# Kernel optimization log

Measured on AMD Instinct MI355X. Metric: run time of the kernel, lower is better.

The kernel has to match this reference:

```python
import jax, jax.numpy as jnp
import numpy as np

N_NODES = 100000
N_EDGES = 1600000
IN_N, IN_E = 128, 64
OUT_N, OUT_E, H = 16, 16, 4


def setup_inputs() -> dict:
    key = jax.random.key(0)
    ks = jax.random.split(key, 11)
    s = 0.05
    return {
        'nfeats': jax.random.normal(ks[0], (N_NODES, IN_N), jnp.float32),
        'efeats': jax.random.normal(ks[1], (N_EDGES, IN_E), jnp.float32),
        'src': jax.random.randint(ks[2], (N_EDGES,), 0, N_NODES, jnp.int32),
        'dst': jax.random.randint(ks[3], (N_EDGES,), 0, N_NODES, jnp.int32),
        'W_ni': jax.random.normal(ks[4], (IN_N, H * OUT_E), jnp.float32) * s,
        'W_nj': jax.random.normal(ks[5], (IN_N, H * OUT_E), jnp.float32) * s,
        'W_fij': jax.random.normal(ks[6], (IN_E, H * OUT_E), jnp.float32) * s,
        'W_src': jax.random.normal(ks[7], (IN_N, H * OUT_N), jnp.float32) * s,
        'b_src': jax.random.normal(ks[8], (H * OUT_N,), jnp.float32) * s,
        'attn': jax.random.normal(ks[9], (H, OUT_E), jnp.float32) * s,
        'bias_e': jax.random.normal(ks[10], (H * OUT_E,), jnp.float32) * s,
    }


def reference(nfeats, efeats, src, dst, W_ni, W_nj, W_fij, W_src, b_src, attn, bias_e):
    N = nfeats.shape[0]
    Hh, De = attn.shape
    # edge features: f_ij = leaky_relu(f_ni[src] + f_nj[dst] + fc_fij(efeats) + bias)
    f_ni = nfeats @ W_ni                                   # [N, H*De]
    f_nj = nfeats @ W_nj                                   # [N, H*De]
    f_fij = efeats @ W_fij                                 # [E, H*De]
    f_out = f_ni[src] + f_nj[dst] + f_fij + bias_e         # [E, H*De]
    f_out = jax.nn.leaky_relu(f_out, 0.01).reshape(-1, Hh, De)  # [E, H, De]
    # attention logits and per-destination softmax (edge_softmax)
    e = jnp.einsum('ehd,hd->eh', f_out, attn)              # [E, H]
    m = jax.ops.segment_max(e, dst, num_segments=N)        # [N, H]
    ex = jnp.exp(e - m[dst])
    z = jax.ops.segment_sum(ex, dst, num_segments=N)       # [N, H]
    a = ex / z[dst]                                        # [E, H]
    # message passing: sum_j a_ij * h_src_j
    h_src = (nfeats @ W_src + b_src).reshape(N, Hh, -1)    # [N, H, Dn]
    msg = a[:, :, None] * h_src[src]                       # [E, H, Dn]
    h_out = jax.ops.segment_sum(msg, dst, num_segments=N)  # [N, H, Dn]
    # aggr='mean' over heads
    res_n = h_out.mean(axis=-2)                            # [N, Dn]
    res_e = f_out.mean(axis=-2)                            # [E, De]
    return res_n, res_e
```

## Files before the change

kernel.cpp:

```cpp
#include <hip/hip_runtime.h>

#define N_NODES 100000
#define N_EDGES 1600000

typedef __bf16 bf16x8 __attribute__((ext_vector_type(8)));
typedef float f32x4 __attribute__((ext_vector_type(4)));

__device__ __forceinline__ __bf16 f2bf(float f) { return (__bf16)f; }

__device__ __forceinline__ bf16x8 cvt8(float4 a, float4 b) {
    bf16x8 r;
    r[0] = f2bf(a.x); r[1] = f2bf(a.y); r[2] = f2bf(a.z); r[3] = f2bf(a.w);
    r[4] = f2bf(b.x); r[5] = f2bf(b.y); r[6] = f2bf(b.z); r[7] = f2bf(b.w);
    return r;
}

__global__ __launch_bounds__(192) void k_node(
    const float* __restrict__ nfeats,
    const float* __restrict__ Wni, const float* __restrict__ Wnj,
    const float* __restrict__ Wsrc, const float* __restrict__ bsrc,
    float* __restrict__ fni, float* __restrict__ fnj, float* __restrict__ hsrc) {
    const int wid  = threadIdx.x >> 6;
    const int lane = threadIdx.x & 63;
    const int quad = lane >> 4, n = lane & 15;

    const float* W  = (wid == 0) ? Wni : (wid == 1) ? Wnj : Wsrc;
    float*       out = (wid == 0) ? fni : (wid == 1) ? fnj : hsrc;

    bf16x8 Bf[4][4];
#pragma unroll
    for (int t = 0; t < 4; ++t)
#pragma unroll
        for (int kc = 0; kc < 4; ++kc)
#pragma unroll
            for (int j = 0; j < 8; ++j) {
                int k = kc * 32 + quad * 8 + j;
                Bf[t][kc][j] = f2bf(W[k * 64 + t * 16 + n]);
            }
    float bs[4];
#pragma unroll
    for (int t = 0; t < 4; ++t) bs[t] = (wid == 2) ? bsrc[t * 16 + n] : 0.0f;

    for (int chunk = blockIdx.x; chunk < N_NODES / 16; chunk += gridDim.x) {
        const int n0 = chunk * 16;
        const float* ap = nfeats + (n0 + n) * 128 + quad * 8;
        bf16x8 Af[4];
#pragma unroll
        for (int kc = 0; kc < 4; ++kc) {
            float4 a0 = *(const float4*)(ap + kc * 32);
            float4 a1 = *(const float4*)(ap + kc * 32 + 4);
            Af[kc] = cvt8(a0, a1);
        }
#pragma unroll
        for (int t = 0; t < 4; ++t) {
            f32x4 acc = {0.f, 0.f, 0.f, 0.f};
#pragma unroll
            for (int kc = 0; kc < 4; ++kc)
                acc = __builtin_amdgcn_mfma_f32_16x16x32_bf16(Af[kc], Bf[t][kc], acc, 0, 0, 0);
#pragma unroll
            for (int reg = 0; reg < 4; ++reg) {
                int row = quad * 4 + reg;
                out[(n0 + row) * 64 + t * 16 + n] = acc[reg] + bs[t];
            }
        }
    }
}

__global__ __launch_bounds__(256) void k_edge1(
    const float* __restrict__ efeats,
    const int* __restrict__ src, const int* __restrict__ dst,
    const float* __restrict__ Wf, const float* __restrict__ biasE,
    const float* __restrict__ attn,
    const float* __restrict__ fni, const float* __restrict__ fnj,
    float* __restrict__ rese, float* __restrict__ exw, float* __restrict__ z) {
    __shared__ float shF[4][16][68];
    const int wid  = threadIdx.x >> 6;
    const int lane = threadIdx.x & 63;
    const int quad = lane >> 4, dcol = lane & 15;

    bf16x8 Bf[4][2];
#pragma unroll
    for (int t = 0; t < 4; ++t)
#pragma unroll
        for (int q = 0; q < 2; ++q)
#pragma unroll
            for (int j = 0; j < 8; ++j) {
                int k = q * 32 + quad * 8 + j;
                Bf[t][q][j] = f2bf(Wf[k * 64 + t * 16 + dcol]);
            }
    float bias_r[4];
#pragma unroll
    for (int h = 0; h < 4; ++h) bias_r[h] = biasE[h * 16 + dcol];

    const int h4 = lane & 3, el = lane >> 2;
    float atr[16];
#pragma unroll
    for (int i = 0; i < 16; ++i) atr[i] = attn[h4 * 16 + i];

    const int nchunk = N_EDGES / 16;
    const int wgid = blockIdx.x * 4 + wid;
    const int nw   = gridDim.x * 4;
    for (int chunk = wgid; chunk < nchunk; chunk += nw) {
        const int e0 = chunk * 16;
        const float* ap = efeats + (e0 + dcol) * 64 + quad * 8;
        bf16x8 af0 = cvt8(*(const float4*)ap, *(const float4*)(ap + 4));
        bf16x8 af1 = cvt8(*(const float4*)(ap + 32), *(const float4*)(ap + 36));
        f32x4 acc[4];
#pragma unroll
        for (int t = 0; t < 4; ++t) {
            f32x4 c0 = {0.f, 0.f, 0.f, 0.f};
            c0     = __builtin_amdgcn_mfma_f32_16x16x32_bf16(af0, Bf[t][0], c0, 0, 0, 0);
            acc[t] = __builtin_amdgcn_mfma_f32_16x16x32_bf16(af1, Bf[t][1], c0, 0, 0, 0);
        }
#pragma unroll
        for (int reg = 0; reg < 4; ++reg) {
            const int row = quad * 4 + reg;
            const int er  = e0 + row;
            const int s = src[er], dd = dst[er];
            const float* pni = fni + s * 64 + dcol;
            const float* pnj = fnj + dd * 64 + dcol;
            float re = 0.f;
#pragma unroll
            for (int h = 0; h < 4; ++h) {
                float v = acc[h][reg] + pni[h * 16] + pnj[h * 16] + bias_r[h];
                v = (v > 0.f) ? v : 0.01f * v;
                re += v;
                shF[wid][row][h * 16 + dcol] = v;
            }
            rese[er * 16 + dcol] = 0.25f * re;
        }
        const float* pf = &shF[wid][el][h4 * 16];
        float4 b0 = *(const float4*)pf;
        float4 b1 = *(const float4*)(pf + 4);
        float4 b2 = *(const float4*)(pf + 8);
        float4 b3 = *(const float4*)(pf + 12);
        float eh = b0.x * atr[0]  + b0.y * atr[1]  + b0.z * atr[2]  + b0.w * atr[3]
                 + b1.x * atr[4]  + b1.y * atr[5]  + b1.z * atr[6]  + b1.w * atr[7]
                 + b2.x * atr[8]  + b2.y * atr[9]  + b2.z * atr[10] + b2.w * atr[11]
                 + b3.x * atr[12] + b3.y * atr[13] + b3.z * atr[14] + b3.w * atr[15];
        float exv = __expf(eh);
        exw[e0 * 4 + lane] = exv;
        const int de = dst[e0 + el];
        atomicAdd(&z[de * 4 + h4], exv);
    }
}

__global__ __launch_bounds__(256) void k_edge2(
    const float* __restrict__ exw, const float* __restrict__ z,
    const int* __restrict__ src, const int* __restrict__ dst,
    const float* __restrict__ hsrc, float* __restrict__ resn) {
    const long total  = (long)N_EDGES * 16;
    const long stride = (long)gridDim.x * blockDim.x;
    for (long i = (long)blockIdx.x * blockDim.x + threadIdx.x; i < total; i += stride) {
        const int e = (int)(i >> 4);
        const int d = (int)(i & 15);
        const float4 exv = *(const float4*)(exw + e * 4);
        const int dn = dst[e], sn = src[e];
        const float4 zv = *(const float4*)(z + dn * 4);
        const float* hp = hsrc + sn * 64 + d;
        float v = exv.x * __builtin_amdgcn_rcpf(zv.x) * hp[0]
                + exv.y * __builtin_amdgcn_rcpf(zv.y) * hp[16]
                + exv.z * __builtin_amdgcn_rcpf(zv.z) * hp[32]
                + exv.w * __builtin_amdgcn_rcpf(zv.w) * hp[48];
        atomicAdd(resn + dn * 16 + d, 0.25f * v);
    }
}

extern "C" void kernel_launch(void* const* d_in, const int* in_sizes, int n_in,
                              void* d_out, int out_size, void* d_ws, size_t ws_size,
                              hipStream_t stream) {
    const float* nfeats = (const float*)d_in[0];
    const float* efeats = (const float*)d_in[1];
    const int*   src    = (const int*)d_in[2];
    const int*   dst    = (const int*)d_in[3];
    const float* W_ni   = (const float*)d_in[4];
    const float* W_nj   = (const float*)d_in[5];
    const float* W_fij  = (const float*)d_in[6];
    const float* W_src  = (const float*)d_in[7];
    const float* b_src  = (const float*)d_in[8];
    const float* attn   = (const float*)d_in[9];
    const float* bias_e = (const float*)d_in[10];

    float* resn = (float*)d_out;
    float* rese = resn + (size_t)N_NODES * 16;

    float* ws   = (float*)d_ws;
    float* fni  = ws;
    float* fnj  = fni  + (size_t)N_NODES * 64;
    float* hsrc = fnj  + (size_t)N_NODES * 64;
    float* exw  = hsrc + (size_t)N_NODES * 64;
    float* z    = exw  + (size_t)N_EDGES * 4;

    hipMemsetAsync(z, 0, (size_t)N_NODES * 4 * sizeof(float), stream);
    hipMemsetAsync(resn, 0, (size_t)N_NODES * 16 * sizeof(float), stream);

    k_node<<<1024, 192, 0, stream>>>(nfeats, W_ni, W_nj, W_src, b_src, fni, fnj, hsrc);
    k_edge1<<<4096, 256, 0, stream>>>(efeats, src, dst, W_fij, bias_e, attn,
                                      fni, fnj, rese, exw, z);
    k_edge2<<<8192, 256, 0, stream>>>(exw, z, src, dst, hsrc, resn);
}
```

Baseline: 812.6 us.

## Build CSR by destination and replace atomic scatter with pull aggregation

Adds a per-call CSR build (degree count, three-stage scan, atomic fill producing a permutation and sorted sources) so that per-destination softmax normalisation and message aggregation run as a pull kernel with one wave per node. The edge kernel now writes exp weights into CSR order instead of doing atomic z accumulation, and the 16-wide atomic scatter of k_edge2 is removed. The softmax denominator is computed in the pull loop. In exchange the change adds five small kernels, scattered atomic writes during the fill, and an irregular exw write in edge1.

```diff
diff --git a/kernel.cpp b/kernel.cpp
--- a/kernel.cpp
+++ b/kernel.cpp
@@ -13,6 +13,84 @@
     r[0] = f2bf(a.x); r[1] = f2bf(a.y); r[2] = f2bf(a.z); r[3] = f2bf(a.w);
     r[4] = f2bf(b.x); r[5] = f2bf(b.y); r[6] = f2bf(b.z); r[7] = f2bf(b.w);
     return r;
+}
+
+__global__ __launch_bounds__(256) void k_deg(const int* __restrict__ dst,
+                                             int* __restrict__ deg) {
+    int e = blockIdx.x * 256 + threadIdx.x;
+    atomicAdd(&deg[dst[e]], 1);
+}
+
+__global__ __launch_bounds__(256) void k_scanA(const int* __restrict__ deg,
+                                               int* __restrict__ bsum) {
+    __shared__ int sh[256];
+    const int tid = threadIdx.x;
+    int n = blockIdx.x * 256 + tid;
+    sh[tid] = (n < N_NODES) ? deg[n] : 0;
+    __syncthreads();
+#pragma unroll
+    for (int s = 128; s > 0; s >>= 1) {
+        if (tid < s) sh[tid] += sh[tid + s];
+        __syncthreads();
+    }
+    if (tid == 0) bsum[blockIdx.x] = sh[0];
+}
+
+#define NB_SCAN 391
+
+__global__ __launch_bounds__(512) void k_scanB(const int* __restrict__ bsum,
+                                               int* __restrict__ bpre,
+                                               int* __restrict__ row_start) {
+    __shared__ int sh[512];
+    const int tid = threadIdx.x;
+    int v = (tid < NB_SCAN) ? bsum[tid] : 0;
+    sh[tid] = v;
+    __syncthreads();
+#pragma unroll
+    for (int off = 1; off < 512; off <<= 1) {
+        int t = (tid >= off) ? sh[tid - off] : 0;
+        __syncthreads();
+        sh[tid] += t;
+        __syncthreads();
+    }
+    if (tid < NB_SCAN) bpre[tid] = sh[tid] - v;
+    if (tid == 0) row_start[N_NODES] = N_EDGES;
+}
+
+__global__ __launch_bounds__(256) void k_scanC(const int* __restrict__ deg,
+                                               const int* __restrict__ bpre,
+                                               int* __restrict__ row_start,
+                                               int* __restrict__ cursor) {
+    __shared__ int sh[256];
+    const int tid = threadIdx.x;
+    int n = blockIdx.x * 256 + tid;
+    int v = (n < N_NODES) ? deg[n] : 0;
+    sh[tid] = v;
+    __syncthreads();
+#pragma unroll
+    for (int off = 1; off < 256; off <<= 1) {
+        int t = (tid >= off) ? sh[tid - off] : 0;
+        __syncthreads();
+        sh[tid] += t;
+        __syncthreads();
+    }
+    if (n < N_NODES) {
+        int ex = sh[tid] - v + bpre[blockIdx.x];
+        row_start[n] = ex;
+        cursor[n]    = ex;
+    }
+}
+
+__global__ __launch_bounds__(256) void k_fill(const int* __restrict__ src,
+                                              const int* __restrict__ dst,
+                                              int* __restrict__ cursor,
+                                              int* __restrict__ perm,
+                                              int* __restrict__ srcp) {
+    int e = blockIdx.x * 256 + threadIdx.x;
+    int d = dst[e];
+    int pos = atomicAdd(&cursor[d], 1);
+    perm[e] = pos;
+    srcp[pos] = src[e];
 }
 
 __global__ __launch_bounds__(192) void k_node(
@@ -72,7 +150,8 @@
     const float* __restrict__ Wf, const float* __restrict__ biasE,
     const float* __restrict__ attn,
     const float* __restrict__ fni, const float* __restrict__ fnj,
-    float* __restrict__ rese, float* __restrict__ exw, float* __restrict__ z) {
+    const int* __restrict__ perm,
+    float* __restrict__ rese, float* __restrict__ exw) {
     __shared__ float shF[4][16][68];
     const int wid  = threadIdx.x >> 6;
     const int lane = threadIdx.x & 63;
@@ -139,31 +218,39 @@
                  + b2.x * atr[8]  + b2.y * atr[9]  + b2.z * atr[10] + b2.w * atr[11]
                  + b3.x * atr[12] + b3.y * atr[13] + b3.z * atr[14] + b3.w * atr[15];
         float exv = __expf(eh);
-        exw[e0 * 4 + lane] = exv;
-        const int de = dst[e0 + el];
-        atomicAdd(&z[de * 4 + h4], exv);
-    }
-}
-
-__global__ __launch_bounds__(256) void k_edge2(
-    const float* __restrict__ exw, const float* __restrict__ z,
-    const int* __restrict__ src, const int* __restrict__ dst,
-    const float* __restrict__ hsrc, float* __restrict__ resn) {
-    const long total  = (long)N_EDGES * 16;
-    const long stride = (long)gridDim.x * blockDim.x;
-    for (long i = (long)blockIdx.x * blockDim.x + threadIdx.x; i < total; i += stride) {
-        const int e = (int)(i >> 4);
-        const int d = (int)(i & 15);
-        const float4 exv = *(const float4*)(exw + e * 4);
-        const int dn = dst[e], sn = src[e];
-        const float4 zv = *(const float4*)(z + dn * 4);
-        const float* hp = hsrc + sn * 64 + d;
-        float v = exv.x * __builtin_amdgcn_rcpf(zv.x) * hp[0]
-                + exv.y * __builtin_amdgcn_rcpf(zv.y) * hp[16]
-                + exv.z * __builtin_amdgcn_rcpf(zv.z) * hp[32]
-                + exv.w * __builtin_amdgcn_rcpf(zv.w) * hp[48];
-        atomicAdd(resn + dn * 16 + d, 0.25f * v);
-    }
+        int p = perm[e0 + el];
+        exw[p * 4 + h4] = exv;
+    }
+}
+
+__global__ __launch_bounds__(256) void k_pull(
+    const int* __restrict__ row_start, const int* __restrict__ srcp,
+    const float* __restrict__ exw, const float* __restrict__ hsrc,
+    float* __restrict__ resn) {
+    const int wid  = threadIdx.x >> 6;
+    const int lane = threadIdx.x & 63;
+    const int h = lane >> 4;
+    const int n = blockIdx.x * 4 + wid;
+    const int start = row_start[n], end = row_start[n + 1];
+    float sacc = 0.f, zacc = 0.f;
+    int i = start;
+    for (; i + 2 <= end; i += 2) {
+        int sn0 = srcp[i], sn1 = srcp[i + 1];
+        float ex0 = exw[i * 4 + h], ex1 = exw[i * 4 + 4 + h];
+        float v0 = hsrc[sn0 * 64 + lane], v1 = hsrc[sn1 * 64 + lane];
+        sacc += ex0 * v0 + ex1 * v1;
+        zacc += ex0 + ex1;
+    }
+    if (i < end) {
+        int sn0 = srcp[i];
+        float ex0 = exw[i * 4 + h];
+        sacc += ex0 * hsrc[sn0 * 64 + lane];
+        zacc += ex0;
+    }
+    float v = (end > start) ? sacc * __builtin_amdgcn_rcpf(zacc) : 0.f;
+    v += __shfl_xor(v, 16, 64);
+    v += __shfl_xor(v, 32, 64);
+    if (lane < 16) resn[n * 16 + lane] = 0.25f * v;
 }
 
 extern "C" void kernel_launch(void* const* d_in, const int* in_sizes, int n_in,
@@ -189,13 +276,25 @@
     float* fnj  = fni  + (size_t)N_NODES * 64;
     float* hsrc = fnj  + (size_t)N_NODES * 64;
     float* exw  = hsrc + (size_t)N_NODES * 64;
-    float* z    = exw  + (size_t)N_EDGES * 4;
-
-    hipMemsetAsync(z, 0, (size_t)N_NODES * 4 * sizeof(float), stream);
-    hipMemsetAsync(resn, 0, (size_t)N_NODES * 16 * sizeof(float), stream);
-
-    k_node<<<1024, 192, 0, stream>>>(nfeats, W_ni, W_nj, W_src, b_src, fni, fnj, hsrc);
+    int*   iws  = (int*)(exw + (size_t)N_EDGES * 4);
+    int* deg       = iws;
+    int* cursor    = deg + N_NODES;
+    int* row_start = cursor + N_NODES;
+    int* perm      = row_start + N_NODES + 1;
+    int* srcp      = perm + N_EDGES;
+    int* bsum      = srcp + N_EDGES;
+    int* bpre      = bsum + NB_SCAN;
+
+    hipMemsetAsync(deg, 0, (size_t)N_NODES * sizeof(int), stream);
+
+    k_deg  <<<N_EDGES / 256, 256, 0, stream>>>(dst, deg);
+    k_scanA<<<NB_SCAN, 256, 0, stream>>>(deg, bsum);
+    k_scanB<<<1, 512, 0, stream>>>(bsum, bpre, row_start);
+    k_scanC<<<NB_SCAN, 256, 0, stream>>>(deg, bpre, row_start, cursor);
+    k_fill <<<N_EDGES / 256, 256, 0, stream>>>(src, dst, cursor, perm, srcp);
+
+    k_node <<<1024, 192, 0, stream>>>(nfeats, W_ni, W_nj, W_src, b_src, fni, fnj, hsrc);
     k_edge1<<<4096, 256, 0, stream>>>(efeats, src, dst, W_fij, bias_e, attn,
-                                      fni, fnj, rese, exw, z);
-    k_edge2<<<8192, 256, 0, stream>>>(exw, z, src, dst, hsrc, resn);
-}
+                                      fni, fnj, perm, rese, exw);
+    k_pull <<<N_NODES / 4, 256, 0, stream>>>(row_start, srcp, exw, hsrc, resn);
+}
```

Result: slower. 1.029 ms (+26.7%).
